# Optimization experiments

Hardware: AMD Instinct MI355X
Metric: run time of the kernel (lower is better)

Reference implementation:

```python
import jax, jax.numpy as jnp
import numpy as np

RADIUS = 0.25
NUM_NEIGHBORS = 32
POS_DIM = 24
STEM_C = 64
PATCH_C = 256
LN_EPS = 1e-5


def query_ball_point(radius, nsample, xyz, new_xyz):
    # xyz: [B,N,3], new_xyz: [B,S,3] -> idx [B,S,nsample] (PointNet++ ball query)
    N = xyz.shape[1]
    sqr = (jnp.sum(new_xyz ** 2, -1)[:, :, None]
           + jnp.sum(xyz ** 2, -1)[:, None, :]
           - 2.0 * jnp.einsum('bsd,bnd->bsn', new_xyz, xyz))  # [B,S,N]
    idx = jnp.broadcast_to(jnp.arange(N, dtype=jnp.int32), sqr.shape)
    idx = jnp.where(sqr > radius * radius, N, idx)
    idx = jnp.sort(idx, axis=-1)[..., :nsample]  # first nsample in-ball (by index order)
    first = idx[..., :1]
    idx = jnp.where(idx == N, first, idx)  # pad empty slots with first neighbor
    return idx


def index_points(points, idx):
    # points [B,N,C], idx [B,S,K] -> [B,S,K,C]
    return jax.vmap(lambda p, i: p[i])(points, idx)


def rel_pos_encoding(rel_xyz, dim=POS_DIM):
    # sinusoidal Fourier encoding of 3D offsets: 3 coords * 2 (sin,cos) * dim//6 freqs
    nf = dim // 6
    freqs = 2.0 ** jnp.arange(nf, dtype=rel_xyz.dtype)
    ang = rel_xyz[..., None] * freqs  # [...,3,nf]
    enc = jnp.concatenate([jnp.sin(ang), jnp.cos(ang)], axis=-1)  # [...,3,2nf]
    return enc.reshape(rel_xyz.shape[:-1] + (dim,))


def point_mlp(x, W, b, gamma, beta, activate):
    h = jnp.einsum('...i,io->...o', x, W) + b
    mu = jnp.mean(h, -1, keepdims=True)
    var = jnp.mean((h - mu) ** 2, -1, keepdims=True)
    h = (h - mu) * jax.lax.rsqrt(var + LN_EPS) * gamma + beta
    return jax.nn.gelu(h, approximate=False) if activate else h


def setup_inputs() -> dict:
    key = jax.random.key(0)
    ks = jax.random.split(key, 8)
    B, N, S = 8, 16384, 1024
    in_c = STEM_C + 3 + POS_DIM  # 91
    return {
        'xyz': jax.random.uniform(ks[0], (B, N, 3), dtype=jnp.float32),
        'point_feature': jax.random.normal(ks[1], (B, N, STEM_C), dtype=jnp.float32),
        'patch_center': jax.random.uniform(ks[2], (B, S, 3), dtype=jnp.float32),
        'W1': jax.random.normal(ks[3], (in_c, PATCH_C), dtype=jnp.float32) * 0.02,
        'b1': jnp.zeros((PATCH_C,), jnp.float32),
        'g1': jnp.ones((PATCH_C,), jnp.float32),
        'be1': jnp.zeros((PATCH_C,), jnp.float32),
        'W2': jax.random.normal(ks[4], (PATCH_C, PATCH_C), dtype=jnp.float32) * 0.02,
        'b2': jnp.zeros((PATCH_C,), jnp.float32),
        'g2': jnp.ones((PATCH_C,), jnp.float32),
        'be2': jnp.zeros((PATCH_C,), jnp.float32),
    }


def reference(xyz, point_feature, patch_center, W1, b1, g1, be1, W2, b2, g2, be2):
    neighbor_idx = query_ball_point(RADIUS, NUM_NEIGHBORS, xyz, patch_center)  # [B,S,K]
    grouped_xyz = index_points(xyz, neighbor_idx)              # [B,S,K,3]
    grouped_feature = index_points(point_feature, neighbor_idx)  # [B,S,K,C]
    relative_xyz = grouped_xyz - patch_center[:, :, None, :]
    relative_position = rel_pos_encoding(relative_xyz)         # [B,S,K,24]
    grouped_input = jnp.concatenate((grouped_feature, relative_xyz, relative_position), axis=-1)
    h = point_mlp(grouped_input, W1, b1, g1, be1, True)
    h = point_mlp(h, W2, b2, g2, be2, False)
    patch_feature = jnp.max(h, axis=2)                         # max over neighbors -> [B,S,PATCH_C]
    return patch_feature, neighbor_idx
```

## Files before the change

kernel.cpp:

```cpp
#include <hip/hip_runtime.h>
#include <math.h>

#define NPTS 16384
#define KN 32
#define C 256
#define NQ 8192
#define PF_ELEMS (NQ * C)

#define W1P_ELEMS (3 * 16 * 64 * 8)
#define W2P_ELEMS (8 * 16 * 64 * 8)
#define WP_ELEMS  (W1P_ELEMS + W2P_ELEMS)
#define HSTR 264

typedef _Float16 half8 __attribute__((ext_vector_type(8)));
typedef _Float16 half4v __attribute__((ext_vector_type(4)));
typedef _Float16 half2t __attribute__((ext_vector_type(2)));
typedef float f32x4 __attribute__((ext_vector_type(4)));

union H8u { half8 v; half2t h2[4]; };

__device__ __forceinline__ float fdot2f(half2t a, half2t b, float c) {
#if __has_builtin(__builtin_amdgcn_fdot2)
    return __builtin_amdgcn_fdot2(a, b, c, false);
#else
    return fmaf((float)a[1], (float)b[1], fmaf((float)a[0], (float)b[0], c));
#endif
}

__device__ __forceinline__ float gelu_tanh(float x) {
    const float t  = x * x;
    const float p2 = fmaf(t, 0.0713548162726f, 1.59576912161f);
    const float e  = __expf(x * p2);
    return x - x * __builtin_amdgcn_rcpf(e + 1.0f);
}

__device__ __forceinline__ void stat8(const H8u& u, half2t ones, float& s, float& s2) {
    #pragma unroll
    for (int j = 0; j < 4; ++j) {
        s  = fdot2f(u.h2[j], ones, s);
        s2 = fdot2f(u.h2[j], u.h2[j], s2);
    }
}

__device__ __forceinline__ void norm_gelu8(H8u& u, const H8u& g, const H8u& be,
                                           half2t rsh, half2t nmuh) {
    #pragma unroll
    for (int j = 0; j < 4; ++j) {
        const half2t A = g.h2[j] * rsh;
        const half2t B = A * nmuh + be.h2[j];
        const half2t y = u.h2[j] * A + B;
        half2t o;
        o[0] = (_Float16)gelu_tanh((float)y[0]);
        o[1] = (_Float16)gelu_tanh((float)y[1]);
        u.h2[j] = o;
    }
}

__device__ __forceinline__ void norm8(H8u& u, const H8u& g, const H8u& be,
                                      half2t rsh, half2t nmuh) {
    #pragma unroll
    for (int j = 0; j < 4; ++j) {
        const half2t A = g.h2[j] * rsh;
        const half2t B = A * nmuh + be.h2[j];
        u.h2[j] = u.h2[j] * A + B;
    }
}

__global__ void prep_kernel(const float* __restrict__ W1,
                            const float* __restrict__ b1,
                            const float* __restrict__ W2,
                            const float* __restrict__ xyz,
                            _Float16* __restrict__ wp,
                            float4* __restrict__ xyzw) {
    const int idx = blockIdx.x * 256 + threadIdx.x;
    if (idx < 96 * 256) {
        const int k = idx >> 8, n = idx & 255;
        const float v = (k < 91) ? W1[k * 256 + n] : ((k == 91) ? b1[n] : 0.0f);
        const int kt = k >> 5, quad = (k >> 3) & 3, j = k & 7;
        const int nt = n >> 4, l15 = n & 15;
        wp[(((kt * 16 + nt) * 64) + quad * 16 + l15) * 8 + j] = (_Float16)v;
    } else if (idx < WP_ELEMS) {
        const int e = idx - 96 * 256;
        const int k = e >> 8, n = e & 255;
        const int kt = k >> 5, quad = (k >> 3) & 3, j = k & 7;
        const int nt = n >> 4, l15 = n & 15;
        wp[W1P_ELEMS + (((kt * 16 + nt) * 64) + quad * 16 + l15) * 8 + j] =
            (_Float16)W2[k * 256 + n];
    } else {
        const int pi = idx - WP_ELEMS;
        const float px = xyz[pi * 3 + 0];
        const float py = xyz[pi * 3 + 1];
        const float pz = xyz[pi * 3 + 2];
        const float sp = __fadd_rn(__fadd_rn(__fmul_rn(px, px), __fmul_rn(py, py)),
                                   __fmul_rn(pz, pz));
        xyzw[pi] = make_float4(px, py, pz, sp);
    }
}

__global__ void __launch_bounds__(256, 8)
encoder_fused(const float4* __restrict__ xyzw,
              const float* __restrict__ pf,
              const float* __restrict__ ctr,
              const float* __restrict__ g1, const float* __restrict__ be1,
              const float* __restrict__ b2, const float* __restrict__ g2,
              const float* __restrict__ be2,
              const _Float16* __restrict__ w1p,
              const _Float16* __restrict__ w2p,
              float* __restrict__ out0,
              float* __restrict__ out1) {
    const int q = blockIdx.x;
    const int b = q >> 10;
    const int t = threadIdx.x;
    const int w = t >> 6;
    const int lane = t & 63;
    const int quad = lane >> 4;
    const int l15  = lane & 15;

    __shared__ __align__(16) unsigned char H16raw[KN * HSTR * 2];
    __shared__ __align__(16) _Float16 lnph[4 * 256];
    __shared__ int nbr[KN];
    __shared__ int wcnt[2][4];

    _Float16 (*H16)[HSTR] = (_Float16(*)[HSTR])H16raw;
    _Float16 (*Xs)[104]   = (_Float16(*)[104])H16raw;
    _Float16* g1h  = lnph;
    _Float16* be1h = lnph + 256;
    _Float16* g2h  = lnph + 512;
    _Float16* be2h = lnph + 768;

    lnph[t]       = (_Float16)g1[t];
    lnph[256 + t] = (_Float16)be1[t];
    lnph[512 + t] = (_Float16)g2[t];
    lnph[768 + t] = (_Float16)be2[t];

    const float4* xwb = xyzw + (size_t)b * NPTS;
    const float cx = ctr[q * 3 + 0];
    const float cy = ctr[q * 3 + 1];
    const float cz = ctr[q * 3 + 2];
    const float sc = __fadd_rn(__fadd_rn(__fmul_rn(cx, cx), __fmul_rn(cy, cy)),
                               __fmul_rn(cz, cz));

    int found = 0;
    int par = 0;
    for (int base = 0; base < NPTS; base += 256) {
        const int n = base + t;
        const float4 pw = xwb[n];
        const float dt = __fadd_rn(__fadd_rn(__fmul_rn(cx, pw.x), __fmul_rn(cy, pw.y)),
                                   __fmul_rn(cz, pw.z));
        const float sqr = __fsub_rn(__fadd_rn(sc, pw.w), __fmul_rn(2.0f, dt));
        const bool inball = (sqr <= 0.0625f);

        const unsigned long long m = __ballot(inball);
        if (lane == 0) wcnt[par][w] = (int)__popcll(m);
        __syncthreads();
        int pre = found;
        if (w > 0) pre += wcnt[par][0];
        if (w > 1) pre += wcnt[par][1];
        if (w > 2) pre += wcnt[par][2];
        const int tot = found + wcnt[par][0] + wcnt[par][1] + wcnt[par][2] + wcnt[par][3];
        const int pos = pre + (int)__popcll(m & ((1ull << lane) - 1ull));
        if (inball && pos < KN) nbr[pos] = n;
        found = tot;
        par ^= 1;
        if (found >= KN) break;
    }
    __syncthreads();
    const int count = (found < KN) ? found : KN;
    const int first = (count > 0) ? nbr[0] : NPTS;

    if (t < KN)
        out1[(size_t)q * KN + t] = (float)((t < count) ? nbr[t] : first);

    {
        const int k  = t >> 3;
        const int tc = t & 7;
        const int nidx = (k < count) ? nbr[k] : first;
        const int n = (nidx < NPTS) ? nidx : NPTS - 1;
        const float4 pw = xwb[n];
        const float rx = pw.x - cx;
        const float ry = pw.y - cy;
        const float rz = pw.z - cz;
        const float* pfr = pf + ((size_t)b * NPTS + n) * 64;

        const float4 f0 = *(const float4*)(pfr + tc * 8);
        const float4 f1 = *(const float4*)(pfr + tc * 8 + 4);
        half8 hv;
        hv[0] = (_Float16)f0.x; hv[1] = (_Float16)f0.y;
        hv[2] = (_Float16)f0.z; hv[3] = (_Float16)f0.w;
        hv[4] = (_Float16)f1.x; hv[5] = (_Float16)f1.y;
        hv[6] = (_Float16)f1.z; hv[7] = (_Float16)f1.w;
        *(half8*)&Xs[k][tc * 8] = hv;

        half4v ov;
        #pragma unroll
        for (int j = 0; j < 4; ++j) {
            const int cm = tc * 4 + j;
            const int jj = cm - 3;
            const int d  = jj >> 3;
            const int mm = jj & 7;
            const float rsel = (d == 0) ? rx : ((d == 1) ? ry : rz);
            const float f2 = __int_as_float(0x3E22F983 + ((mm & 3) << 23));
            const float arg = fmaf(rsel, f2, (mm >= 4) ? 0.25f : 0.0f);
#if __has_builtin(__builtin_amdgcn_sinf)
            const float sv = __builtin_amdgcn_sinf(arg);
#else
            const float sv = __sinf(arg * 6.2831853071795864f);
#endif
            float v = (cm < 3) ? ((cm == 0) ? rx : ((cm == 1) ? ry : rz)) : sv;
            v = (cm == 27) ? 1.0f : ((cm > 27) ? 0.0f : v);
            ov[j] = (_Float16)v;
        }
        *(half4v*)&Xs[k][64 + tc * 4] = ov;
    }
    __syncthreads();

    f32x4 acc[2][4];

    const int wu = __builtin_amdgcn_readfirstlane(w);
    const _Float16* __restrict__ w1w = w1p + (size_t)(wu * 4) * 512;
    const _Float16* __restrict__ w2w = w2p + (size_t)(wu * 4) * 512;
    const int lo8 = lane * 8;

    #pragma unroll
    for (int mt = 0; mt < 2; ++mt)
        #pragma unroll
        for (int nt = 0; nt < 4; ++nt)
            acc[mt][nt] = (f32x4){0.f, 0.f, 0.f, 0.f};

    #pragma unroll
    for (int kt = 0; kt < 3; ++kt) {
        const half8 x0 = *(const half8*)&Xs[l15][kt * 32 + quad * 8];
        const half8 x1 = *(const half8*)&Xs[16 + l15][kt * 32 + quad * 8];
        #pragma unroll
        for (int nt = 0; nt < 4; ++nt) {
            const half8 wf = *(const half8*)(w1w + (kt * 16 + nt) * 512 + lo8);
            acc[0][nt] = __builtin_amdgcn_mfma_f32_16x16x32_f16(wf, x0, acc[0][nt], 0, 0, 0);
            acc[1][nt] = __builtin_amdgcn_mfma_f32_16x16x32_f16(wf, x1, acc[1][nt], 0, 0, 0);
        }
    }
    __syncthreads();

    #pragma unroll
    for (int nt = 0; nt < 4; ++nt) {
        const int chb = (w * 4 + nt) * 16 + quad * 4;
        #pragma unroll
        for (int mt = 0; mt < 2; ++mt) {
            half4v h;
            #pragma unroll
            for (int r = 0; r < 4; ++r)
                h[r] = (_Float16)acc[mt][nt][r];
            *(half4v*)&H16[mt * 16 + l15][chb] = h;
        }
    }
    __syncthreads();

    const int row = t >> 3;
    const int p   = t & 7;
    _Float16* hrow0 = &H16[row][16 * p];
    _Float16* hrow1 = &H16[row][128 + 16 * p];
    half2t ones;
    ones[0] = (_Float16)1.0f;
    ones[1] = (_Float16)1.0f;

    {
        H8u u0, u1, u2, u3;
        u0.v = *(const half8*)hrow0;
        u1.v = *(const half8*)(hrow0 + 8);
        u2.v = *(const half8*)hrow1;
        u3.v = *(const half8*)(hrow1 + 8);

        float s = 0.0f, s2 = 0.0f;
        stat8(u0, ones, s, s2); stat8(u1, ones, s, s2);
        stat8(u2, ones, s, s2); stat8(u3, ones, s, s2);
        #pragma unroll
        for (int off = 1; off < 8; off <<= 1) {
            s  += __shfl_xor(s, off, 64);
            s2 += __shfl_xor(s2, off, 64);
        }
        const float mu  = s * (1.0f / 256.0f);
        const float var = fmaf(s2, 1.0f / 256.0f, -mu * mu);
        const float rs  = __builtin_amdgcn_rsqf(var + 1e-5f);
        half2t rsh, nmuh;
        rsh[0]  = (_Float16)rs;    rsh[1]  = (_Float16)rs;
        nmuh[0] = (_Float16)(-mu); nmuh[1] = (_Float16)(-mu);

        H8u gA0, gA1, gB0, gB1, bA0, bA1, bB0, bB1;
        gA0.v = *(const half8*)&g1h[16 * p];        bA0.v = *(const half8*)&be1h[16 * p];
        gA1.v = *(const half8*)&g1h[16 * p + 8];    bA1.v = *(const half8*)&be1h[16 * p + 8];
        gB0.v = *(const half8*)&g1h[128 + 16 * p];  bB0.v = *(const half8*)&be1h[128 + 16 * p];
        gB1.v = *(const half8*)&g1h[136 + 16 * p];  bB1.v = *(const half8*)&be1h[136 + 16 * p];

        norm_gelu8(u0, gA0, bA0, rsh, nmuh);
        norm_gelu8(u1, gA1, bA1, rsh, nmuh);
        norm_gelu8(u2, gB0, bB0, rsh, nmuh);
        norm_gelu8(u3, gB1, bB1, rsh, nmuh);

        *(half8*)hrow0       = u0.v;
        *(half8*)(hrow0 + 8) = u1.v;
        *(half8*)hrow1       = u2.v;
        *(half8*)(hrow1 + 8) = u3.v;
    }
    __syncthreads();

    #pragma unroll
    for (int mt = 0; mt < 2; ++mt)
        #pragma unroll
        for (int nt = 0; nt < 4; ++nt)
            acc[mt][nt] = (f32x4){0.f, 0.f, 0.f, 0.f};

    #pragma unroll
    for (int kt = 0; kt < 8; ++kt) {
        const half8 h0 = *(const half8*)&H16[l15][kt * 32 + quad * 8];
        const half8 h1 = *(const half8*)&H16[16 + l15][kt * 32 + quad * 8];
        #pragma unroll
        for (int nt = 0; nt < 4; ++nt) {
            const half8 wf = *(const half8*)(w2w + (kt * 16 + nt) * 512 + lo8);
            acc[0][nt] = __builtin_amdgcn_mfma_f32_16x16x32_f16(wf, h0, acc[0][nt], 0, 0, 0);
            acc[1][nt] = __builtin_amdgcn_mfma_f32_16x16x32_f16(wf, h1, acc[1][nt], 0, 0, 0);
        }
    }
    __syncthreads();

    #pragma unroll
    for (int nt = 0; nt < 4; ++nt) {
        const int chb = (w * 4 + nt) * 16 + quad * 4;
        const f32x4 bv = *(const f32x4*)&b2[chb];
        #pragma unroll
        for (int mt = 0; mt < 2; ++mt) {
            half4v h;
            #pragma unroll
            for (int r = 0; r < 4; ++r)
                h[r] = (_Float16)(acc[mt][nt][r] + bv[r]);
            *(half4v*)&H16[mt * 16 + l15][chb] = h;
        }
    }
    __syncthreads();

    {
        H8u u0, u1, u2, u3;
        u0.v = *(const half8*)hrow0;
        u1.v = *(const half8*)(hrow0 + 8);
        u2.v = *(const half8*)hrow1;
        u3.v = *(const half8*)(hrow1 + 8);

        float s = 0.0f, s2 = 0.0f;
        stat8(u0, ones, s, s2); stat8(u1, ones, s, s2);
        stat8(u2, ones, s, s2); stat8(u3, ones, s, s2);
        #pragma unroll
        for (int off = 1; off < 8; off <<= 1) {
            s  += __shfl_xor(s, off, 64);
            s2 += __shfl_xor(s2, off, 64);
        }
        const float mu  = s * (1.0f / 256.0f);
        const float var = fmaf(s2, 1.0f / 256.0f, -mu * mu);
        const float rs  = __builtin_amdgcn_rsqf(var + 1e-5f);
        half2t rsh, nmuh;
        rsh[0]  = (_Float16)rs;    rsh[1]  = (_Float16)rs;
        nmuh[0] = (_Float16)(-mu); nmuh[1] = (_Float16)(-mu);

        H8u gA0, gA1, gB0, gB1, bA0, bA1, bB0, bB1;
        gA0.v = *(const half8*)&g2h[16 * p];        bA0.v = *(const half8*)&be2h[16 * p];
        gA1.v = *(const half8*)&g2h[16 * p + 8];    bA1.v = *(const half8*)&be2h[16 * p + 8];
        gB0.v = *(const half8*)&g2h[128 + 16 * p];  bB0.v = *(const half8*)&be2h[128 + 16 * p];
        gB1.v = *(const half8*)&g2h[136 + 16 * p];  bB1.v = *(const half8*)&be2h[136 + 16 * p];

        norm8(u0, gA0, bA0, rsh, nmuh);
        norm8(u1, gA1, bA1, rsh, nmuh);
        norm8(u2, gB0, bB0, rsh, nmuh);
        norm8(u3, gB1, bB1, rsh, nmuh);

        *(half8*)hrow0       = u0.v;
        *(half8*)(hrow0 + 8) = u1.v;
        *(half8*)hrow1       = u2.v;
        *(half8*)(hrow1 + 8) = u3.v;
    }
    __syncthreads();

    if (t < 128) {
        const _Float16* Hf = &H16[0][0];
        half2t mx = *(const half2t*)(Hf + 2 * t);
        #pragma unroll
        for (int r = 1; r < KN; ++r) {
            const half2t v = *(const half2t*)(Hf + r * HSTR + 2 * t);
            mx = __builtin_elementwise_max(mx, v);
        }
        float2 o2;
        o2.x = (float)mx[0];
        o2.y = (float)mx[1];
        *(float2*)&out0[(size_t)q * C + 2 * t] = o2;
    }
}

extern "C" void kernel_launch(void* const* d_in, const int* in_sizes, int n_in,
                              void* d_out, int out_size, void* d_ws, size_t ws_size,
                              hipStream_t stream) {
    const float* xyz = (const float*)d_in[0];
    const float* pf  = (const float*)d_in[1];
    const float* ctr = (const float*)d_in[2];
    const float* W1  = (const float*)d_in[3];
    const float* b1  = (const float*)d_in[4];
    const float* g1  = (const float*)d_in[5];
    const float* be1 = (const float*)d_in[6];
    const float* W2  = (const float*)d_in[7];
    const float* b2  = (const float*)d_in[8];
    const float* g2  = (const float*)d_in[9];
    const float* be2 = (const float*)d_in[10];

    float* out = (float*)d_out;
    _Float16* wp = (_Float16*)d_ws;
    float4* xyzw = (float4*)(wp + WP_ELEMS);

    prep_kernel<<<(WP_ELEMS + NPTS * 8) / 256, 256, 0, stream>>>(W1, b1, W2, xyz, wp, xyzw);
    encoder_fused<<<NQ, 256, 0, stream>>>(xyzw, pf, ctr,
                                          g1, be1, b2, g2, be2,
                                          wp, wp + W1P_ELEMS,
                                          out, out + PF_ELEMS);
}
```

Measured before the change: 188.4 us.

## Compute LayerNorm stats from MFMA accumulators and prefetch ball-query points

The LayerNorm mean and variance are now computed directly from the MFMA accumulator registers, reduced with shuffles plus a small shared-memory cross-wave table. Normalization and GELU are then applied before the single fp16 store to shared memory, which removes a store/reload round trip and one barrier per layer. The ball query now handles 512 points per iteration with software-prefetched loads. The point buffer is padded with far-away sentinel points so the prefetch never reads out of bounds. Stats are now taken in fp32 from unrounded values, which shifts numerics slightly, and the larger query stride may scan more points than strictly needed.

```diff
diff --git a/kernel.cpp b/kernel.cpp
--- a/kernel.cpp
+++ b/kernel.cpp
@@ -2,6 +2,7 @@
 #include <math.h>
 
 #define NPTS 16384
+#define NPTS_PAD 16896
 #define KN 32
 #define C 256
 #define NQ 8192
@@ -10,60 +11,19 @@
 #define W1P_ELEMS (3 * 16 * 64 * 8)
 #define W2P_ELEMS (8 * 16 * 64 * 8)
 #define WP_ELEMS  (W1P_ELEMS + W2P_ELEMS)
+#define XYZW_ELEMS (8 * NPTS_PAD)
 #define HSTR 264
 
 typedef _Float16 half8 __attribute__((ext_vector_type(8)));
 typedef _Float16 half4v __attribute__((ext_vector_type(4)));
 typedef _Float16 half2t __attribute__((ext_vector_type(2)));
 typedef float f32x4 __attribute__((ext_vector_type(4)));
-
-union H8u { half8 v; half2t h2[4]; };
-
-__device__ __forceinline__ float fdot2f(half2t a, half2t b, float c) {
-#if __has_builtin(__builtin_amdgcn_fdot2)
-    return __builtin_amdgcn_fdot2(a, b, c, false);
-#else
-    return fmaf((float)a[1], (float)b[1], fmaf((float)a[0], (float)b[0], c));
-#endif
-}
 
 __device__ __forceinline__ float gelu_tanh(float x) {
     const float t  = x * x;
     const float p2 = fmaf(t, 0.0713548162726f, 1.59576912161f);
     const float e  = __expf(x * p2);
     return x - x * __builtin_amdgcn_rcpf(e + 1.0f);
-}
-
-__device__ __forceinline__ void stat8(const H8u& u, half2t ones, float& s, float& s2) {
-    #pragma unroll
-    for (int j = 0; j < 4; ++j) {
-        s  = fdot2f(u.h2[j], ones, s);
-        s2 = fdot2f(u.h2[j], u.h2[j], s2);
-    }
-}
-
-__device__ __forceinline__ void norm_gelu8(H8u& u, const H8u& g, const H8u& be,
-                                           half2t rsh, half2t nmuh) {
-    #pragma unroll
-    for (int j = 0; j < 4; ++j) {
-        const half2t A = g.h2[j] * rsh;
-        const half2t B = A * nmuh + be.h2[j];
-        const half2t y = u.h2[j] * A + B;
-        half2t o;
-        o[0] = (_Float16)gelu_tanh((float)y[0]);
-        o[1] = (_Float16)gelu_tanh((float)y[1]);
-        u.h2[j] = o;
-    }
-}
-
-__device__ __forceinline__ void norm8(H8u& u, const H8u& g, const H8u& be,
-                                      half2t rsh, half2t nmuh) {
-    #pragma unroll
-    for (int j = 0; j < 4; ++j) {
-        const half2t A = g.h2[j] * rsh;
-        const half2t B = A * nmuh + be.h2[j];
-        u.h2[j] = u.h2[j] * A + B;
-    }
 }
 
 __global__ void prep_kernel(const float* __restrict__ W1,
@@ -87,13 +47,21 @@
         wp[W1P_ELEMS + (((kt * 16 + nt) * 64) + quad * 16 + l15) * 8 + j] =
             (_Float16)W2[k * 256 + n];
     } else {
-        const int pi = idx - WP_ELEMS;
-        const float px = xyz[pi * 3 + 0];
-        const float py = xyz[pi * 3 + 1];
-        const float pz = xyz[pi * 3 + 2];
-        const float sp = __fadd_rn(__fadd_rn(__fmul_rn(px, px), __fmul_rn(py, py)),
-                                   __fmul_rn(pz, pz));
-        xyzw[pi] = make_float4(px, py, pz, sp);
+        const int e  = idx - WP_ELEMS;
+        const int bb = e / NPTS_PAD;
+        const int off = e - bb * NPTS_PAD;
+        float4 v;
+        if (off < NPTS) {
+            const float px = xyz[((size_t)bb * NPTS + off) * 3 + 0];
+            const float py = xyz[((size_t)bb * NPTS + off) * 3 + 1];
+            const float pz = xyz[((size_t)bb * NPTS + off) * 3 + 2];
+            const float sp = __fadd_rn(__fadd_rn(__fmul_rn(px, px), __fmul_rn(py, py)),
+                                       __fmul_rn(pz, pz));
+            v = make_float4(px, py, pz, sp);
+        } else {
+            v = make_float4(1e9f, 1e9f, 1e9f, 3e18f);
+        }
+        xyzw[(size_t)bb * NPTS_PAD + off] = v;
     }
 }
 
@@ -118,8 +86,9 @@
 
     __shared__ __align__(16) unsigned char H16raw[KN * HSTR * 2];
     __shared__ __align__(16) _Float16 lnph[4 * 256];
+    __shared__ __align__(16) float2 sred[2][16][4];
     __shared__ int nbr[KN];
-    __shared__ int wcnt[2][4];
+    __shared__ int wcnt[2][2][4];
 
     _Float16 (*H16)[HSTR] = (_Float16(*)[HSTR])H16raw;
     _Float16 (*Xs)[104]   = (_Float16(*)[104])H16raw;
@@ -133,36 +102,61 @@
     lnph[512 + t] = (_Float16)g2[t];
     lnph[768 + t] = (_Float16)be2[t];
 
-    const float4* xwb = xyzw + (size_t)b * NPTS;
+    const float4* xwb = xyzw + (size_t)b * NPTS_PAD;
     const float cx = ctr[q * 3 + 0];
     const float cy = ctr[q * 3 + 1];
     const float cz = ctr[q * 3 + 2];
     const float sc = __fadd_rn(__fadd_rn(__fmul_rn(cx, cx), __fmul_rn(cy, cy)),
                                __fmul_rn(cz, cz));
 
+    float4 pw0 = xwb[t];
+    float4 pw1 = xwb[256 + t];
     int found = 0;
     int par = 0;
-    for (int base = 0; base < NPTS; base += 256) {
-        const int n = base + t;
-        const float4 pw = xwb[n];
-        const float dt = __fadd_rn(__fadd_rn(__fmul_rn(cx, pw.x), __fmul_rn(cy, pw.y)),
-                                   __fmul_rn(cz, pw.z));
-        const float sqr = __fsub_rn(__fadd_rn(sc, pw.w), __fmul_rn(2.0f, dt));
-        const bool inball = (sqr <= 0.0625f);
-
-        const unsigned long long m = __ballot(inball);
-        if (lane == 0) wcnt[par][w] = (int)__popcll(m);
+    for (int base = 0; base < NPTS; base += 512) {
+        const float4 nx0 = xwb[base + 512 + t];
+        const float4 nx1 = xwb[base + 768 + t];
+
+        const float dt0 = __fadd_rn(__fadd_rn(__fmul_rn(cx, pw0.x), __fmul_rn(cy, pw0.y)),
+                                    __fmul_rn(cz, pw0.z));
+        const float sq0 = __fsub_rn(__fadd_rn(sc, pw0.w), __fmul_rn(2.0f, dt0));
+        const float dt1 = __fadd_rn(__fadd_rn(__fmul_rn(cx, pw1.x), __fmul_rn(cy, pw1.y)),
+                                    __fmul_rn(cz, pw1.z));
+        const float sq1 = __fsub_rn(__fadd_rn(sc, pw1.w), __fmul_rn(2.0f, dt1));
+        const bool in0 = (sq0 <= 0.0625f);
+        const bool in1 = (sq1 <= 0.0625f);
+
+        const unsigned long long m0 = __ballot(in0);
+        const unsigned long long m1 = __ballot(in1);
+        if (lane == 0) {
+            wcnt[par][0][w] = (int)__popcll(m0);
+            wcnt[par][1][w] = (int)__popcll(m1);
+        }
         __syncthreads();
-        int pre = found;
-        if (w > 0) pre += wcnt[par][0];
-        if (w > 1) pre += wcnt[par][1];
-        if (w > 2) pre += wcnt[par][2];
-        const int tot = found + wcnt[par][0] + wcnt[par][1] + wcnt[par][2] + wcnt[par][3];
-        const int pos = pre + (int)__popcll(m & ((1ull << lane) - 1ull));
-        if (inball && pos < KN) nbr[pos] = n;
-        found = tot;
+        const int c00 = wcnt[par][0][0], c01 = wcnt[par][0][1];
+        const int c02 = wcnt[par][0][2], c03 = wcnt[par][0][3];
+        const int c10 = wcnt[par][1][0], c11 = wcnt[par][1][1];
+        const int c12 = wcnt[par][1][2], c13 = wcnt[par][1][3];
+        int pre0 = found;
+        if (w > 0) pre0 += c00;
+        if (w > 1) pre0 += c01;
+        if (w > 2) pre0 += c02;
+        const int C0 = c00 + c01 + c02 + c03;
+        int pre1 = found + C0;
+        if (w > 0) pre1 += c10;
+        if (w > 1) pre1 += c11;
+        if (w > 2) pre1 += c12;
+        const int tot = C0 + c10 + c11 + c12 + c13;
+        const unsigned long long lmask = (1ull << lane) - 1ull;
+        const int pos0 = pre0 + (int)__popcll(m0 & lmask);
+        const int pos1 = pre1 + (int)__popcll(m1 & lmask);
+        if (in0 && pos0 < KN) nbr[pos0] = base + t;
+        if (in1 && pos1 < KN) nbr[pos1] = base + 256 + t;
+        found += tot;
         par ^= 1;
         if (found >= KN) break;
+        pw0 = nx0;
+        pw1 = nx1;
     }
     __syncthreads();
     const int count = (found < KN) ? found : KN;
@@ -238,67 +232,58 @@
             acc[1][nt] = __builtin_amdgcn_mfma_f32_16x16x32_f16(wf, x1, acc[1][nt], 0, 0, 0);
         }
     }
-    __syncthreads();
+
+    float mu0, mu1, rs0, rs1;
+    {
+        #pragma unroll
+        for (int mt = 0; mt < 2; ++mt) {
+            float s = 0.0f, s2 = 0.0f;
+            #pragma unroll
+            for (int nt = 0; nt < 4; ++nt)
+                #pragma unroll
+                for (int r = 0; r < 4; ++r) {
+                    const float v = acc[mt][nt][r];
+                    s += v;
+                    s2 = fmaf(v, v, s2);
+                }
+            s  += __shfl_xor(s, 16, 64);  s  += __shfl_xor(s, 32, 64);
+            s2 += __shfl_xor(s2, 16, 64); s2 += __shfl_xor(s2, 32, 64);
+            if (quad == 0) sred[mt][l15][w] = make_float2(s, s2);
+        }
+    }
+    __syncthreads();
+    {
+        #pragma unroll
+        for (int mt = 0; mt < 2; ++mt) {
+            const float4 pA = *(const float4*)&sred[mt][l15][0];
+            const float4 pB = *(const float4*)&sred[mt][l15][2];
+            const float S = pA.x + pA.z + pB.x + pB.z;
+            const float Q = pA.y + pA.w + pB.y + pB.w;
+            const float mu = S * (1.0f / 256.0f);
+            const float var = fmaf(Q, 1.0f / 256.0f, -mu * mu);
+            const float rs = __builtin_amdgcn_rsqf(var + 1e-5f);
+            if (mt == 0) { mu0 = mu; rs0 = rs; } else { mu1 = mu; rs1 = rs; }
+        }
+    }
 
     #pragma unroll
     for (int nt = 0; nt < 4; ++nt) {
         const int chb = (w * 4 + nt) * 16 + quad * 4;
-        #pragma unroll
-        for (int mt = 0; mt < 2; ++mt) {
+        const half4v g4h  = *(const half4v*)&g1h[chb];
+        const half4v be4h = *(const half4v*)&be1h[chb];
+        #pragma unroll
+        for (int mt = 0; mt < 2; ++mt) {
+            const float mu = (mt == 0) ? mu0 : mu1;
+            const float rs = (mt == 0) ? rs0 : rs1;
             half4v h;
             #pragma unroll
-            for (int r = 0; r < 4; ++r)
-                h[r] = (_Float16)acc[mt][nt][r];
+            for (int r = 0; r < 4; ++r) {
+                const float A = (float)g4h[r] * rs;
+                const float y = fmaf(acc[mt][nt][r] - mu, A, (float)be4h[r]);
+                h[r] = (_Float16)gelu_tanh(y);
+            }
             *(half4v*)&H16[mt * 16 + l15][chb] = h;
         }
-    }
-    __syncthreads();
-
-    const int row = t >> 3;
-    const int p   = t & 7;
-    _Float16* hrow0 = &H16[row][16 * p];
-    _Float16* hrow1 = &H16[row][128 + 16 * p];
-    half2t ones;
-    ones[0] = (_Float16)1.0f;
-    ones[1] = (_Float16)1.0f;
-
-    {
-        H8u u0, u1, u2, u3;
-        u0.v = *(const half8*)hrow0;
-        u1.v = *(const half8*)(hrow0 + 8);
-        u2.v = *(const half8*)hrow1;
-        u3.v = *(const half8*)(hrow1 + 8);
-
-        float s = 0.0f, s2 = 0.0f;
-        stat8(u0, ones, s, s2); stat8(u1, ones, s, s2);
-        stat8(u2, ones, s, s2); stat8(u3, ones, s, s2);
-        #pragma unroll
-        for (int off = 1; off < 8; off <<= 1) {
-            s  += __shfl_xor(s, off, 64);
-            s2 += __shfl_xor(s2, off, 64);
-        }
-        const float mu  = s * (1.0f / 256.0f);
-        const float var = fmaf(s2, 1.0f / 256.0f, -mu * mu);
-        const float rs  = __builtin_amdgcn_rsqf(var + 1e-5f);
-        half2t rsh, nmuh;
-        rsh[0]  = (_Float16)rs;    rsh[1]  = (_Float16)rs;
-        nmuh[0] = (_Float16)(-mu); nmuh[1] = (_Float16)(-mu);
-
-        H8u gA0, gA1, gB0, gB1, bA0, bA1, bB0, bB1;
-        gA0.v = *(const half8*)&g1h[16 * p];        bA0.v = *(const half8*)&be1h[16 * p];
-        gA1.v = *(const half8*)&g1h[16 * p + 8];    bA1.v = *(const half8*)&be1h[16 * p + 8];
-        gB0.v = *(const half8*)&g1h[128 + 16 * p];  bB0.v = *(const half8*)&be1h[128 + 16 * p];
-        gB1.v = *(const half8*)&g1h[136 + 16 * p];  bB1.v = *(const half8*)&be1h[136 + 16 * p];
-
-        norm_gelu8(u0, gA0, bA0, rsh, nmuh);
-        norm_gelu8(u1, gA1, bA1, rsh, nmuh);
-        norm_gelu8(u2, gB0, bB0, rsh, nmuh);
-        norm_gelu8(u3, gB1, bB1, rsh, nmuh);
-
-        *(half8*)hrow0       = u0.v;
-        *(half8*)(hrow0 + 8) = u1.v;
-        *(half8*)hrow1       = u2.v;
-        *(half8*)(hrow1 + 8) = u3.v;
     }
     __syncthreads();
 
@@ -319,60 +304,65 @@
             acc[1][nt] = __builtin_amdgcn_mfma_f32_16x16x32_f16(wf, h1, acc[1][nt], 0, 0, 0);
         }
     }
-    __syncthreads();
+
+    #pragma unroll
+    for (int nt = 0; nt < 4; ++nt) {
+        const f32x4 bv = *(const f32x4*)&b2[(w * 4 + nt) * 16 + quad * 4];
+        #pragma unroll
+        for (int mt = 0; mt < 2; ++mt)
+            #pragma unroll
+            for (int r = 0; r < 4; ++r)
+                acc[mt][nt][r] += bv[r];
+    }
+    {
+        #pragma unroll
+        for (int mt = 0; mt < 2; ++mt) {
+            float s = 0.0f, s2 = 0.0f;
+            #pragma unroll
+            for (int nt = 0; nt < 4; ++nt)
+                #pragma unroll
+                for (int r = 0; r < 4; ++r) {
+                    const float v = acc[mt][nt][r];
+                    s += v;
+                    s2 = fmaf(v, v, s2);
+                }
+            s  += __shfl_xor(s, 16, 64);  s  += __shfl_xor(s, 32, 64);
+            s2 += __shfl_xor(s2, 16, 64); s2 += __shfl_xor(s2, 32, 64);
+            if (quad == 0) sred[mt][l15][w] = make_float2(s, s2);
+        }
+    }
+    __syncthreads();
+    {
+        #pragma unroll
+        for (int mt = 0; mt < 2; ++mt) {
+            const float4 pA = *(const float4*)&sred[mt][l15][0];
+            const float4 pB = *(const float4*)&sred[mt][l15][2];
+            const float S = pA.x + pA.z + pB.x + pB.z;
+            const float Q = pA.y + pA.w + pB.y + pB.w;
+            const float mu = S * (1.0f / 256.0f);
+            const float var = fmaf(Q, 1.0f / 256.0f, -mu * mu);
+            const float rs = __builtin_amdgcn_rsqf(var + 1e-5f);
+            if (mt == 0) { mu0 = mu; rs0 = rs; } else { mu1 = mu; rs1 = rs; }
+        }
+    }
 
     #pragma unroll
     for (int nt = 0; nt < 4; ++nt) {
         const int chb = (w * 4 + nt) * 16 + quad * 4;
-        const f32x4 bv = *(const f32x4*)&b2[chb];
-        #pragma unroll
-        for (int mt = 0; mt < 2; ++mt) {
+        const half4v g4h  = *(const half4v*)&g2h[chb];
+        const half4v be4h = *(const half4v*)&be2h[chb];
+        #pragma unroll
+        for (int mt = 0; mt < 2; ++mt) {
+            const float mu = (mt == 0) ? mu0 : mu1;
+            const float rs = (mt == 0) ? rs0 : rs1;
             half4v h;
             #pragma unroll
-            for (int r = 0; r < 4; ++r)
-                h[r] = (_Float16)(acc[mt][nt][r] + bv[r]);
+            for (int r = 0; r < 4; ++r) {
+                const float A = (float)g4h[r] * rs;
+                h[r] = (_Float16)fmaf(acc[mt][nt][r] - mu, A, (float)be4h[r]);
+            }
             *(half4v*)&H16[mt * 16 + l15][chb] = h;
         }
-    }
-    __syncthreads();
-
-    {
-        H8u u0, u1, u2, u3;
-        u0.v = *(const half8*)hrow0;
-        u1.v = *(const half8*)(hrow0 + 8);
-        u2.v = *(const half8*)hrow1;
-        u3.v = *(const half8*)(hrow1 + 8);
-
-        float s = 0.0f, s2 = 0.0f;
-        stat8(u0, ones, s, s2); stat8(u1, ones, s, s2);
-        stat8(u2, ones, s, s2); stat8(u3, ones, s, s2);
-        #pragma unroll
-        for (int off = 1; off < 8; off <<= 1) {
-            s  += __shfl_xor(s, off, 64);
-            s2 += __shfl_xor(s2, off, 64);
-        }
-        const float mu  = s * (1.0f / 256.0f);
-        const float var = fmaf(s2, 1.0f / 256.0f, -mu * mu);
-        const float rs  = __builtin_amdgcn_rsqf(var + 1e-5f);
-        half2t rsh, nmuh;
-        rsh[0]  = (_Float16)rs;    rsh[1]  = (_Float16)rs;
-        nmuh[0] = (_Float16)(-mu); nmuh[1] = (_Float16)(-mu);
-
-        H8u gA0, gA1, gB0, gB1, bA0, bA1, bB0, bB1;
-        gA0.v = *(const half8*)&g2h[16 * p];        bA0.v = *(const half8*)&be2h[16 * p];
-        gA1.v = *(const half8*)&g2h[16 * p + 8];    bA1.v = *(const half8*)&be2h[16 * p + 8];
-        gB0.v = *(const half8*)&g2h[128 + 16 * p];  bB0.v = *(const half8*)&be2h[128 + 16 * p];
-        gB1.v = *(const half8*)&g2h[136 + 16 * p];  bB1.v = *(const half8*)&be2h[136 + 16 * p];
-
-        norm8(u0, gA0, bA0, rsh, nmuh);
-        norm8(u1, gA1, bA1, rsh, nmuh);
-        norm8(u2, gB0, bB0, rsh, nmuh);
-        norm8(u3, gB1, bB1, rsh, nmuh);
-
-        *(half8*)hrow0       = u0.v;
-        *(half8*)(hrow0 + 8) = u1.v;
-        *(half8*)hrow1       = u2.v;
-        *(half8*)(hrow1 + 8) = u3.v;
     }
     __syncthreads();
 
@@ -410,7 +400,7 @@
     _Float16* wp = (_Float16*)d_ws;
     float4* xyzw = (float4*)(wp + WP_ELEMS);
 
-    prep_kernel<<<(WP_ELEMS + NPTS * 8) / 256, 256, 0, stream>>>(W1, b1, W2, xyz, wp, xyzw);
+    prep_kernel<<<(WP_ELEMS + XYZW_ELEMS) / 256, 256, 0, stream>>>(W1, b1, W2, xyz, wp, xyzw);
     encoder_fused<<<NQ, 256, 0, stream>>>(xyzw, pf, ctr,
                                           g1, be1, b2, g2, be2,
                                           wp, wp + W1P_ELEMS,
```

Result: no change. 186.7 us (-0.9%).
